# Performance work log

Hardware: AMD Instinct MI355X
Metric: run time of the kernel (lower is better)

The kernel has to match this reference:

```python
import jax
import jax.numpy as jnp
import numpy as np

# Config mirroring GLOBAL_CONFIG['attn'] / kernel config in the source
BM = 64            # query-group (block) size; asserted 64 or 192 in source
TOP_KEYS = 0.1     # fraction of keys kept via top-k on colsum scores
MULTIPLE_OF = 64   # counts_multiple_of: indices_count rounded to this
LW1D = 0.15        # local_1d_window fraction
RAND_INV_PROB = 100

B, H, N, D = 1, 12, 2048, 128


def setup_inputs() -> dict:
    key = jax.random.key(0)
    kq, kk, kv, kc = jax.random.split(key, 4)
    shape = (B, H, N, D)
    q = jax.random.normal(kq, shape, dtype=jnp.float32)
    k = jax.random.normal(kk, shape, dtype=jnp.float32)
    v = jax.random.normal(kv, shape, dtype=jnp.float32)
    out_cache = jax.random.normal(kc, shape, dtype=jnp.float32)
    return {"q": q, "k": k, "v": v, "out_cache": out_cache}


def _static_1d_mask(n: int, bm: int, lw1d: float) -> jnp.ndarray:
    # initialize_1d_static_mask: per query-group local window centered at
    # qg*bm + bm//2, width int(lw1d*n), clipped to [0, n). Shape [qg, n].
    qg = n // bm
    ws = int(lw1d * n)
    centers = jnp.arange(qg) * bm + bm // 2          # [qg]
    j = jnp.arange(n)                                  # [n]
    lo = centers[:, None] - ws // 2
    hi = centers[:, None] + ws // 2
    return (j[None, :] >= lo) & (j[None, :] < hi)


def _scatter_true(mask, idx):
    # mask.scatter_(-1, idx, True) along last axis
    K = idx.shape[-1]
    n = mask.shape[-1]
    flat = mask.reshape(-1, n)
    fidx = idx.reshape(-1, K)
    rows = jnp.arange(flat.shape[0])[:, None]
    flat = flat.at[rows, fidx].set(True)
    return flat.reshape(mask.shape)


def _sparse_diff_attn(q, k, v, out_cache):
    b, h, n, d = q.shape
    qg = n // BM
    scale = 1.0 / jnp.sqrt(jnp.asarray(d, q.dtype))
    # dense scores (dense_colsum_attn computes these on the full step)
    scores = jnp.einsum('bhid,bhjd->bhij', q, k) * scale   # [b,h,n,n]
    probs = jax.nn.softmax(scores, axis=-1)
    # bs: column-sum of attention probabilities per query group  [b,h,qg,n]
    bs = probs.reshape(b, h, qg, BM, n).sum(axis=3)
    # indices_count = multiple_of * round(top_keys * n / multiple_of)
    indices_count = MULTIPLE_OF * int(round(TOP_KEYS * n / MULTIPLE_OF))
    rmask = jax.random.randint(jax.random.key(1), bs.shape, 0, RAND_INV_PROB) == 0
    _, idx = jax.lax.top_k(bs, indices_count)
    mask = _scatter_true(rmask, idx)                       # [b,h,qg,n]
    static = _static_1d_mask(n, BM, LW1D)                  # [qg,n]
    # video_query_groups: groups where static window + topk still sparse
    vqg = (static.sum(axis=-1, keepdims=True) + indices_count) < n  # [qg,1]
    mask = mask & vqg[None, None]
    mask = mask | static[None, None]
    # csp_attn: block-sparse attention; every query i in group i//BM attends
    # only to keys selected in mask[.., i//BM, :]
    full_mask = jnp.repeat(mask, BM, axis=2)               # [b,h,n,n]
    sp_scores = jnp.where(full_mask, scores, -jnp.inf)
    sp_probs = jax.nn.softmax(sp_scores, axis=-1)
    sp_out = jnp.einsum('bhij,bhjd->bhid', sp_probs, v)
    # sparse step: o = o_cache + csp_attn(...)  (sign = +1)
    return out_cache + sp_out


def reference(q, k, v, out_cache):
    return _sparse_diff_attn(q, k, v, out_cache)
```

## Files before the change

### kernel.cpp

```cpp
#include <hip/hip_runtime.h>
#include <math.h>

constexpr int Hh   = 12;
constexpr int Nn   = 2048;
constexpr int Dd   = 128;
constexpr int BMq  = 64;
constexpr int QGg  = 32;
constexpr int KSEL = 192;
constexpr int CK   = 32;
constexpr float SCALE = 0.08838834764831845f;

typedef _Float16 v8h __attribute__((ext_vector_type(8)));
typedef float    v4f __attribute__((ext_vector_type(4)));

__device__ __attribute__((aligned(16))) _Float16 g_qh[(size_t)Hh*Nn*Dd];
__device__ __attribute__((aligned(16))) _Float16 g_ql[(size_t)Hh*Nn*Dd];
__device__ __attribute__((aligned(16))) _Float16 g_kh[(size_t)Hh*Nn*Dd];
__device__ __attribute__((aligned(16))) _Float16 g_kl[(size_t)Hh*Nn*Dd];
__device__ float          g_lp[(size_t)Hh*Nn*16];
__device__ float          g_bs[(size_t)Hh*QGg*Nn];
__device__ unsigned short g_sel[Hh*QGg*Nn];
__device__ int            g_cnt[Hh*QGg];

__device__ __forceinline__ unsigned int rotl32(unsigned int x, int n){
  return (x << n) | (x >> (32 - n));
}

__device__ __forceinline__ unsigned pack2h(_Float16 a, _Float16 b){
  unsigned short ua, ub;
  __builtin_memcpy(&ua, &a, 2);
  __builtin_memcpy(&ub, &b, 2);
  return (unsigned)ua | ((unsigned)ub << 16);
}

__device__ __forceinline__ void tf2x32(unsigned int k0, unsigned int k1,
                                       unsigned int x0, unsigned int x1,
                                       unsigned int &o0, unsigned int &o1){
  const unsigned int ks2 = 0x1BD11BDAu ^ k0 ^ k1;
  x0 += k0; x1 += k1;
  x0 += x1; x1 = rotl32(x1,13); x1 ^= x0;
  x0 += x1; x1 = rotl32(x1,15); x1 ^= x0;
  x0 += x1; x1 = rotl32(x1,26); x1 ^= x0;
  x0 += x1; x1 = rotl32(x1, 6); x1 ^= x0;
  x0 += k1; x1 += ks2 + 1u;
  x0 += x1; x1 = rotl32(x1,17); x1 ^= x0;
  x0 += x1; x1 = rotl32(x1,29); x1 ^= x0;
  x0 += x1; x1 = rotl32(x1,16); x1 ^= x0;
  x0 += x1; x1 = rotl32(x1,24); x1 ^= x0;
  x0 += ks2; x1 += k0 + 2u;
  x0 += x1; x1 = rotl32(x1,13); x1 ^= x0;
  x0 += x1; x1 = rotl32(x1,15); x1 ^= x0;
  x0 += x1; x1 = rotl32(x1,26); x1 ^= x0;
  x0 += x1; x1 = rotl32(x1, 6); x1 ^= x0;
  x0 += k0; x1 += k1 + 3u;
  x0 += x1; x1 = rotl32(x1,17); x1 ^= x0;
  x0 += x1; x1 = rotl32(x1,29); x1 ^= x0;
  x0 += x1; x1 = rotl32(x1,16); x1 ^= x0;
  x0 += x1; x1 = rotl32(x1,24); x1 ^= x0;
  x0 += k1; x1 += ks2 + 4u;
  x0 += x1; x1 = rotl32(x1,13); x1 ^= x0;
  x0 += x1; x1 = rotl32(x1,15); x1 ^= x0;
  x0 += x1; x1 = rotl32(x1,26); x1 ^= x0;
  x0 += x1; x1 = rotl32(x1, 6); x1 ^= x0;
  x0 += ks2; x1 += k0 + 5u;
  o0 = x0; o1 = x1;
}

__device__ __forceinline__ bool jax_rand01(unsigned int idx,
                                           unsigned int k1a, unsigned int k1b,
                                           unsigned int k2a, unsigned int k2b){
  unsigned int h0, h1, l0, l1;
  tf2x32(k1a, k1b, 0u, idx, h0, h1);
  tf2x32(k2a, k2b, 0u, idx, l0, l1);
  unsigned int h = h0 ^ h1;
  unsigned int l = l0 ^ l1;
  unsigned int off = ((h % 100u) * 96u + (l % 100u)) % 100u;
  return off == 0u;
}

__global__ __launch_bounds__(256) void k0_cvt(const float* __restrict__ Q,
                                              const float* __restrict__ K){
  const int bid = blockIdx.x;
  const int t = threadIdx.x;
  const int kc = t >> 6, ln = t & 63;
  const int row = ln & 15;
  const int col = kc*32 + (ln >> 4)*8;
  const size_t src = ((size_t)bid*16 + row)*Dd + col;
  const size_t ob  = (((size_t)bid)*4 + kc)*512 + (size_t)ln*8;

  float4 qa = *(const float4*)(Q + src);
  float4 qb = *(const float4*)(Q + src + 4);
  float qs[8] = {qa.x*SCALE, qa.y*SCALE, qa.z*SCALE, qa.w*SCALE,
                 qb.x*SCALE, qb.y*SCALE, qb.z*SCALE, qb.w*SCALE};
  v8h qh, ql;
  #pragma unroll
  for (int j = 0; j < 8; ++j){
    _Float16 hi = (_Float16)qs[j];
    qh[j] = hi;
    ql[j] = (_Float16)(qs[j] - (float)hi);
  }
  *(v8h*)&g_qh[ob] = qh;
  *(v8h*)&g_ql[ob] = ql;

  float4 ka = *(const float4*)(K + src);
  float4 kb = *(const float4*)(K + src + 4);
  float ks[8] = {ka.x, ka.y, ka.z, ka.w, kb.x, kb.y, kb.z, kb.w};
  v8h kh, kl;
  #pragma unroll
  for (int j = 0; j < 8; ++j){
    _Float16 hi = (_Float16)ks[j];
    kh[j] = hi;
    kl[j] = (_Float16)(ks[j] - (float)hi);
  }
  *(v8h*)&g_kh[ob] = kh;
  *(v8h*)&g_kl[ob] = kl;
}

__global__ __launch_bounds__(256) void k1_rowsum(){
  const int bid0 = blockIdx.x;
  const int w = (bid0 & 7)*384 + (bid0 >> 3);
  const int jb = w & 15, gp = (w >> 4) & 15, h = w >> 8;
  const int t = threadIdx.x;
  const int wv = t >> 6, ln = t & 63;
  const int nidx = ln & 15, quad = ln >> 4;
  const size_t lnoff = (size_t)ln*8;
  const size_t habase = ((size_t)h*128 + gp*8 + wv*2)*4;
  const size_t hbbase = ((size_t)h*128 + jb*8)*4;

  v4f acc[2][8];
  #pragma unroll
  for (int tr = 0; tr < 2; ++tr)
    #pragma unroll
    for (int tc = 0; tc < 8; ++tc)
      acc[tr][tc] = (v4f){0.f, 0.f, 0.f, 0.f};

  for (int kc = 0; kc < 4; ++kc){
    v8h ahi[2], alo[2];
    #pragma unroll
    for (int tr = 0; tr < 2; ++tr){
      const size_t ab = (habase + tr*4 + kc)*512 + lnoff;
      ahi[tr] = *(const v8h*)&g_qh[ab];
      alo[tr] = *(const v8h*)&g_ql[ab];
    }
    v8h bhi[8], blo[8];
    #pragma unroll
    for (int tc = 0; tc < 8; ++tc){
      const size_t bb = (hbbase + tc*4 + kc)*512 + lnoff;
      bhi[tc] = *(const v8h*)&g_kh[bb];
      blo[tc] = *(const v8h*)&g_kl[bb];
    }
    #pragma unroll
    for (int tr = 0; tr < 2; ++tr)
      #pragma unroll
      for (int tc = 0; tc < 8; ++tc){
        acc[tr][tc] = __builtin_amdgcn_mfma_f32_16x16x32_f16(ahi[tr], bhi[tc], acc[tr][tc], 0, 0, 0);
        acc[tr][tc] = __builtin_amdgcn_mfma_f32_16x16x32_f16(ahi[tr], blo[tc], acc[tr][tc], 0, 0, 0);
        acc[tr][tc] = __builtin_amdgcn_mfma_f32_16x16x32_f16(alo[tr], bhi[tc], acc[tr][tc], 0, 0, 0);
      }
  }

  #pragma unroll
  for (int tr = 0; tr < 2; ++tr){
    float rs[4] = {0.f, 0.f, 0.f, 0.f};
    #pragma unroll
    for (int tc = 0; tc < 8; ++tc){
      #pragma unroll
      for (int r = 0; r < 4; ++r){
        rs[r] += __expf(acc[tr][tc][r]);
      }
    }
    #pragma unroll
    for (int r = 0; r < 4; ++r){
      float v = rs[r];
      v += __shfl_xor(v, 1);
      v += __shfl_xor(v, 2);
      v += __shfl_xor(v, 4);
      v += __shfl_xor(v, 8);
      rs[r] = v;
    }
    if (nidx == 0){
      #pragma unroll
      for (int r = 0; r < 4; ++r){
        const int row = (wv*2+tr)*16 + quad*4 + r;
        g_lp[((size_t)h*Nn + gp*128 + row)*16 + jb] = rs[r];
      }
    }
  }
}

__global__ __launch_bounds__(256) void k2r_colsum(){
  const int bid0 = blockIdx.x;
  const int w = (bid0 & 7)*384 + (bid0 >> 3);
  const int jb = w & 15, gp = (w >> 4) & 15, h = w >> 8;
  const int t = threadIdx.x;
  const int wv = t >> 6, ln = t & 63;
  const int nidx = ln & 15, quad = ln >> 4;
  const size_t lnoff = (size_t)ln*8;
  const size_t habase = ((size_t)h*128 + gp*8 + wv*2)*4;
  const size_t hbbase = ((size_t)h*128 + jb*8)*4;

  __shared__ float il_s[128];
  __shared__ float part[4][128];
  if (t < 128){
    const float* lp = &g_lp[((size_t)h*Nn + gp*128 + t)*16];
    float s = 0.f;
    #pragma unroll
    for (int x = 0; x < 16; ++x) s += lp[x];
    il_s[t] = 1.0f / s;
  }
  __syncthreads();

  v4f acc[2][8];
  #pragma unroll
  for (int tr = 0; tr < 2; ++tr)
    #pragma unroll
    for (int tc = 0; tc < 8; ++tc)
      acc[tr][tc] = (v4f){0.f, 0.f, 0.f, 0.f};

  for (int kc = 0; kc < 4; ++kc){
    v8h ahi[2], alo[2];
    #pragma unroll
    for (int tr = 0; tr < 2; ++tr){
      const size_t ab = (habase + tr*4 + kc)*512 + lnoff;
      ahi[tr] = *(const v8h*)&g_qh[ab];
      alo[tr] = *(const v8h*)&g_ql[ab];
    }
    v8h bhi[8], blo[8];
    #pragma unroll
    for (int tc = 0; tc < 8; ++tc){
      const size_t bb = (hbbase + tc*4 + kc)*512 + lnoff;
      bhi[tc] = *(const v8h*)&g_kh[bb];
      blo[tc] = *(const v8h*)&g_kl[bb];
    }
    #pragma unroll
    for (int tr = 0; tr < 2; ++tr)
      #pragma unroll
      for (int tc = 0; tc < 8; ++tc){
        acc[tr][tc] = __builtin_amdgcn_mfma_f32_16x16x32_f16(ahi[tr], bhi[tc], acc[tr][tc], 0, 0, 0);
        acc[tr][tc] = __builtin_amdgcn_mfma_f32_16x16x32_f16(ahi[tr], blo[tc], acc[tr][tc], 0, 0, 0);
        acc[tr][tc] = __builtin_amdgcn_mfma_f32_16x16x32_f16(alo[tr], bhi[tc], acc[tr][tc], 0, 0, 0);
      }
  }

  float csg[8];
  #pragma unroll
  for (int tc = 0; tc < 8; ++tc) csg[tc] = 0.f;
  #pragma unroll
  for (int tr = 0; tr < 2; ++tr){
    #pragma unroll
    for (int tc = 0; tc < 8; ++tc){
      float cs = 0.f;
      #pragma unroll
      for (int r = 0; r < 4; ++r){
        const int row = (wv*2+tr)*16 + quad*4 + r;
        cs += __expf(acc[tr][tc][r]) * il_s[row];
      }
      cs += __shfl_xor(cs, 16);
      cs += __shfl_xor(cs, 32);
      csg[tc] += cs;
    }
  }
  if (ln < 16){
    #pragma unroll
    for (int tc = 0; tc < 8; ++tc) part[wv][tc*16 + nidx] = csg[tc];
  }
  __syncthreads();
  const int col = t & 127, grp = t >> 7;
  g_bs[((size_t)h*QGg + gp*2 + grp)*Nn + jb*128 + col] =
      part[grp*2][col] + part[grp*2 + 1][col];
}

__global__ __launch_bounds__(256) void k2b_mask(){
  const int bid = blockIdx.x, g = bid % QGg, t = threadIdx.x;
  const int wv = t >> 6, lw = t & 63;
  __shared__ int hist[256];
  __shared__ int wsum[4];
  __shared__ int selb_s, selgt_s;
  __shared__ int csel;
  __shared__ int eqn;
  __shared__ int eqpos[Nn];
  const float* src = g_bs + (size_t)bid*Nn;
  float mine[8];
  {
    float4 a = *(const float4*)&src[t*4];
    float4 b = *(const float4*)&src[1024 + t*4];
    mine[0]=a.x; mine[1]=a.y; mine[2]=a.z; mine[3]=a.w;
    mine[4]=b.x; mine[5]=b.y; mine[6]=b.z; mine[7]=b.w;
  }
  if (t == 0){ csel = 0; eqn = 0; }
  unsigned int bu8[8];
  #pragma unroll
  for (int u = 0; u < 8; ++u) bu8[u] = __float_as_uint(mine[u]);

  unsigned int k1a, k1b, k2a, k2b;
  tf2x32(0u, 1u, 0u, 0u, k1a, k1b);
  tf2x32(0u, 1u, 0u, 1u, k2a, k2b);

  unsigned int pref = 0u;
  unsigned int msk  = 0u;
  int rem = KSEL;
  #pragma unroll
  for (int pass = 3; pass >= 0; --pass){
    const int shift = pass*8;
    hist[t] = 0;
    __syncthreads();
    #pragma unroll
    for (int u = 0; u < 8; ++u){
      if ((bu8[u] & msk) == pref)
        atomicAdd(&hist[(bu8[u] >> shift) & 0xFFu], 1);
    }
    __syncthreads();
    const int hcnt = hist[t];
    int s = hcnt;
    #pragma unroll
    for (int d = 1; d < 64; d <<= 1){
      int tmp = __shfl_down(s, d);
      if (lw + d < 64) s += tmp;
    }
    if (lw == 0) wsum[wv] = s;
    __syncthreads();
    int base = 0;
    #pragma unroll
    for (int w2 = 1; w2 < 4; ++w2) if (wv + w2 < 4) base += wsum[wv + w2];
    const int gt_incl = s + base;
    const int gt = gt_incl - hcnt;
    if (gt < rem && gt_incl >= rem){ selb_s = t; selgt_s = gt; }
    __syncthreads();
    pref |= ((unsigned)selb_s) << shift;
    msk  |= 0xFFu << shift;
    rem  -= selgt_s;
  }
  const unsigned int T = pref;
  const int need = rem;

  #pragma unroll
  for (int u = 0; u < 8; ++u){
    int j = (u < 4) ? (t*4 + u) : (1024 + t*4 + u - 4);
    if (bu8[u] == T){
      int s = atomicAdd(&eqn, 1);
      eqpos[s] = j;
    }
  }
  __syncthreads();
  const int en = eqn;

  const int lo = g*BMq + BMq/2 - 153;
  const int hi = g*BMq + BMq/2 + 153;
  const int ssum = ((hi < Nn) ? hi : Nn) - ((lo > 0) ? lo : 0);
  const bool vqg = (ssum + KSEL) < Nn;

  #pragma unroll
  for (int u = 0; u < 8; ++u){
    int j = (u < 4) ? (t*4 + u) : (1024 + t*4 + u - 4);
    unsigned int bu = bu8[u];
    bool topk = bu > T;
    if (!topk && bu == T){
      int tr = 0;
      for (int i = 0; i < en; ++i)
        tr += (eqpos[i] < j) ? 1 : 0;
      topk = (tr < need);
    }
    bool rnd = jax_rand01((unsigned)(bid*Nn + j), k1a, k1b, k2a, k2b);
    bool st  = (j >= lo) && (j < hi);
    bool selb = st || ((rnd || topk) && vqg);
    if (selb){
      int slot = atomicAdd(&csel, 1);
      g_sel[(size_t)bid*Nn + slot] = (unsigned short)j;
    }
  }
  __syncthreads();
  if (t == 0) g_cnt[bid] = csel;
}

__global__ __launch_bounds__(256) void k3_attn(const float* __restrict__ K,
                                               const float* __restrict__ V,
                                               const float* __restrict__ OC,
                                               float* __restrict__ out){
  const int bid0 = blockIdx.x;
  const int w    = (bid0 & 7)*96 + (bid0 >> 3);
  const int half = w & 1;
  const int gg   = w >> 1;
  const int h = gg / QGg, g = gg % QGg;
  const int t = threadIdx.x;
  const int wv = t >> 6, ln = t & 63;
  const int nidx = ln & 15, quad = ln >> 4;
  const int qtile = wv >> 1, kdt = wv & 1;

  __shared__ _Float16 kh_s[CK][136];
  __shared__ _Float16 kl_s[CK][136];
  __shared__ _Float16 vTh[Dd][40];
  __shared__ _Float16 vTl[Dd][40];
  __shared__ _Float16 p_h[32][40];
  __shared__ _Float16 p_l[32][40];
  __shared__ float    l_part[2][32];
  __shared__ float    l_s[32];

  const int c = g_cnt[gg];
  const unsigned short* sel = g_sel + (size_t)gg*Nn;

  const int rb = g*4 + half*2 + qtile;
  v8h aHi[4], aLo[4];
  #pragma unroll
  for (int kc = 0; kc < 4; ++kc){
    const size_t ab = (((size_t)h*128 + rb)*4 + kc)*512 + (size_t)ln*8;
    aHi[kc] = *(const v8h*)&g_qh[ab];
    aLo[kc] = *(const v8h*)&g_ql[ab];
  }

  if (t < 64) l_part[t >> 5][t & 31] = 0.0f;

  float4 kreg[4], vreg[4];
  {
    const int cc0 = (c < CK) ? c : CK;
    #pragma unroll
    for (int it = 0; it < 4; ++it){
      int e = it*256 + t, row = e >> 5, c4 = e & 31;
      int j = (row < cc0) ? (int)sel[row] : 0;
      kreg[it] = ((const float4*)(K + ((size_t)h*Nn + j)*Dd))[c4];
      vreg[it] = ((const float4*)(V + ((size_t)h*Nn + j)*Dd))[c4];
    }
  }

  v4f acc[4];
  #pragma unroll
  for (int dt = 0; dt < 4; ++dt) acc[dt] = (v4f){0.f, 0.f, 0.f, 0.f};

  const int cg = (quad ^ ((nidx >> 2) & 3)) * 8;

  for (int c0 = 0; c0 < c; c0 += CK){
    const int cc = ((c - c0) < CK) ? (c - c0) : CK;
    #pragma unroll
    for (int it = 0; it < 4; ++it){
      int e = it*256 + t, row = e >> 5, c4 = e & 31;
      float4 kv = kreg[it];
      float xs[4] = {kv.x, kv.y, kv.z, kv.w};
      _Float16 hh[4], ll[4];
      #pragma unroll
      for (int m = 0; m < 4; ++m){
        _Float16 hi = (_Float16)xs[m];
        hh[m] = hi;
        ll[m] = (_Float16)(xs[m] - (float)hi);
      }
      *(unsigned*)&kh_s[row][c4*4 + 0] = pack2h(hh[0], hh[1]);
      *(unsigned*)&kh_s[row][c4*4 + 2] = pack2h(hh[2], hh[3]);
      *(unsigned*)&kl_s[row][c4*4 + 0] = pack2h(ll[0], ll[1]);
      *(unsigned*)&kl_s[row][c4*4 + 2] = pack2h(ll[2], ll[3]);
      float4 vv = vreg[it];
      float vs[4] = {vv.x, vv.y, vv.z, vv.w};
      const int swz = row ^ ((c4 & 3) << 3);
      #pragma unroll
      for (int m = 0; m < 4; ++m){
        _Float16 hi = (_Float16)vs[m];
        vTh[c4*4 + m][swz] = hi;
        vTl[c4*4 + m][swz] = (_Float16)(vs[m] - (float)hi);
      }
    }
    __syncthreads();
    {
      const int nc0 = c0 + CK;
      if (nc0 < c){
        const int ncc = ((c - nc0) < CK) ? (c - nc0) : CK;
        #pragma unroll
        for (int it = 0; it < 4; ++it){
          int e = it*256 + t, row = e >> 5, c4 = e & 31;
          int j = (row < ncc) ? (int)sel[nc0 + row] : 0;
          kreg[it] = ((const float4*)(K + ((size_t)h*Nn + j)*Dd))[c4];
          vreg[it] = ((const float4*)(V + ((size_t)h*Nn + j)*Dd))[c4];
        }
      }
    }
    v4f sc = (v4f){0.f, 0.f, 0.f, 0.f};
    #pragma unroll
    for (int kc = 0; kc < 4; ++kc){
      v8h bh = *(const v8h*)&kh_s[kdt*16 + nidx][kc*32 + quad*8];
      v8h bl = *(const v8h*)&kl_s[kdt*16 + nidx][kc*32 + quad*8];
      sc = __builtin_amdgcn_mfma_f32_16x16x32_f16(aHi[kc], bh, sc, 0, 0, 0);
      sc = __builtin_amdgcn_mfma_f32_16x16x32_f16(aHi[kc], bl, sc, 0, 0, 0);
      sc = __builtin_amdgcn_mfma_f32_16x16x32_f16(aLo[kc], bh, sc, 0, 0, 0);
    }
    {
      const int k_loc = kdt*16 + nidx;
      float rs[4];
      #pragma unroll
      for (int r = 0; r < 4; ++r){
        float sv = (k_loc < cc) ? __expf(sc[r]) : 0.f;
        rs[r] = sv;
        _Float16 hi = (_Float16)sv;
        const int row = qtile*16 + quad*4 + r;
        p_h[row][k_loc] = hi;
        p_l[row][k_loc] = (_Float16)(sv - (float)hi);
      }
      #pragma unroll
      for (int r = 0; r < 4; ++r){
        float v = rs[r];
        v += __shfl_xor(v, 1);
        v += __shfl_xor(v, 2);
        v += __shfl_xor(v, 4);
        v += __shfl_xor(v, 8);
        rs[r] = v;
      }
      if (nidx == 0){
        #pragma unroll
        for (int r = 0; r < 4; ++r)
          l_part[kdt][qtile*16 + quad*4 + r] += rs[r];
      }
    }
    __syncthreads();
    {
      v8h ph = *(const v8h*)&p_h[qtile*16 + nidx][quad*8];
      v8h pl = *(const v8h*)&p_l[qtile*16 + nidx][quad*8];
      #pragma unroll
      for (int dt = 0; dt < 4; ++dt){
        const int d = (kdt*4 + dt)*16 + nidx;
        v8h vh = *(const v8h*)&vTh[d][cg];
        v8h vl = *(const v8h*)&vTl[d][cg];
        acc[dt] = __builtin_amdgcn_mfma_f32_16x16x32_f16(ph, vh, acc[dt], 0, 0, 0);
        acc[dt] = __builtin_amdgcn_mfma_f32_16x16x32_f16(ph, vl, acc[dt], 0, 0, 0);
        acc[dt] = __builtin_amdgcn_mfma_f32_16x16x32_f16(pl, vh, acc[dt], 0, 0, 0);
      }
    }
    __syncthreads();
  }

  if (t < 32) l_s[t] = 1.0f / (l_part[0][t] + l_part[1][t]);
  __syncthreads();

  #pragma unroll
  for (int dt = 0; dt < 4; ++dt){
    const int d = (kdt*4 + dt)*16 + nidx;
    #pragma unroll
    for (int r = 0; r < 4; ++r){
      const int row = qtile*16 + quad*4 + r;
      const float il = l_s[row];
      const size_t o = ((size_t)h*Nn + (size_t)g*BMq + half*32 + row)*Dd + d;
      out[o] = acc[dt][r]*il + OC[o];
    }
  }
}

extern "C" void kernel_launch(void* const* d_in, const int* in_sizes, int n_in,
                              void* d_out, int out_size, void* d_ws, size_t ws_size,
                              hipStream_t stream) {
  (void)in_sizes; (void)n_in; (void)out_size; (void)d_ws; (void)ws_size;
  const float* Q  = (const float*)d_in[0];
  const float* K  = (const float*)d_in[1];
  const float* V  = (const float*)d_in[2];
  const float* OC = (const float*)d_in[3];
  float* out = (float*)d_out;
  hipLaunchKernelGGL(k0_cvt,     dim3(Hh*128),   dim3(256), 0, stream, Q, K);
  hipLaunchKernelGGL(k1_rowsum,  dim3(Hh*16*16), dim3(256), 0, stream);
  hipLaunchKernelGGL(k2r_colsum, dim3(Hh*16*16), dim3(256), 0, stream);
  hipLaunchKernelGGL(k2b_mask,   dim3(Hh*QGg),   dim3(256), 0, stream);
  hipLaunchKernelGGL(k3_attn,    dim3(Hh*QGg*2), dim3(256), 0, stream, K, V, OC, out);
}
```

Measured before the change: 270.0 us.

## Stage shared K tiles in LDS with double-buffered register prefetch in QK kernels

In both the rowsum and colsum QK^T kernels, each of the four waves used to load the full K hi/lo fragments from global memory on its own. The block now loads them cooperatively into a double-buffered LDS tile, prefetching the next k-chunk into registers while the current one is computed. This cuts redundant global and L2 traffic by a factor of four and frees registers, at the cost of LDS space and one barrier per chunk. The il_s barrier is folded into the loop barriers, with an extra sync before the colsum epilogue.

```diff
diff --git a/kernel.cpp b/kernel.cpp
--- a/kernel.cpp
+++ b/kernel.cpp
@@ -127,6 +127,19 @@
   const size_t habase = ((size_t)h*128 + gp*8 + wv*2)*4;
   const size_t hbbase = ((size_t)h*128 + jb*8)*4;
 
+  __shared__ v8h Bh[2][8][64], Bl[2][8][64];
+  const int f0 = t*2, f1 = t*2 + 1;
+  const int tc0 = f0 >> 6, bln0 = f0 & 63;
+  const int tc1 = f1 >> 6, bln1 = f1 & 63;
+
+  v8h rbh0, rbh1, rbl0, rbl1;
+  {
+    const size_t a0 = (hbbase + tc0*4 + 0)*512 + (size_t)bln0*8;
+    const size_t a1 = (hbbase + tc1*4 + 0)*512 + (size_t)bln1*8;
+    rbh0 = *(const v8h*)&g_kh[a0]; rbh1 = *(const v8h*)&g_kh[a1];
+    rbl0 = *(const v8h*)&g_kl[a0]; rbl1 = *(const v8h*)&g_kl[a1];
+  }
+
   v4f acc[2][8];
   #pragma unroll
   for (int tr = 0; tr < 2; ++tr)
@@ -135,6 +148,16 @@
       acc[tr][tc] = (v4f){0.f, 0.f, 0.f, 0.f};
 
   for (int kc = 0; kc < 4; ++kc){
+    const int cur = kc & 1;
+    Bh[cur][tc0][bln0] = rbh0; Bh[cur][tc1][bln1] = rbh1;
+    Bl[cur][tc0][bln0] = rbl0; Bl[cur][tc1][bln1] = rbl1;
+    __syncthreads();
+    if (kc < 3){
+      const size_t a0 = (hbbase + tc0*4 + kc+1)*512 + (size_t)bln0*8;
+      const size_t a1 = (hbbase + tc1*4 + kc+1)*512 + (size_t)bln1*8;
+      rbh0 = *(const v8h*)&g_kh[a0]; rbh1 = *(const v8h*)&g_kh[a1];
+      rbl0 = *(const v8h*)&g_kl[a0]; rbl1 = *(const v8h*)&g_kl[a1];
+    }
     v8h ahi[2], alo[2];
     #pragma unroll
     for (int tr = 0; tr < 2; ++tr){
@@ -142,21 +165,17 @@
       ahi[tr] = *(const v8h*)&g_qh[ab];
       alo[tr] = *(const v8h*)&g_ql[ab];
     }
-    v8h bhi[8], blo[8];
     #pragma unroll
     for (int tc = 0; tc < 8; ++tc){
-      const size_t bb = (hbbase + tc*4 + kc)*512 + lnoff;
-      bhi[tc] = *(const v8h*)&g_kh[bb];
-      blo[tc] = *(const v8h*)&g_kl[bb];
-    }
-    #pragma unroll
-    for (int tr = 0; tr < 2; ++tr)
-      #pragma unroll
-      for (int tc = 0; tc < 8; ++tc){
-        acc[tr][tc] = __builtin_amdgcn_mfma_f32_16x16x32_f16(ahi[tr], bhi[tc], acc[tr][tc], 0, 0, 0);
-        acc[tr][tc] = __builtin_amdgcn_mfma_f32_16x16x32_f16(ahi[tr], blo[tc], acc[tr][tc], 0, 0, 0);
-        acc[tr][tc] = __builtin_amdgcn_mfma_f32_16x16x32_f16(alo[tr], bhi[tc], acc[tr][tc], 0, 0, 0);
-      }
+      v8h bh = Bh[cur][tc][ln];
+      v8h bl = Bl[cur][tc][ln];
+      #pragma unroll
+      for (int tr = 0; tr < 2; ++tr){
+        acc[tr][tc] = __builtin_amdgcn_mfma_f32_16x16x32_f16(ahi[tr], bh, acc[tr][tc], 0, 0, 0);
+        acc[tr][tc] = __builtin_amdgcn_mfma_f32_16x16x32_f16(ahi[tr], bl, acc[tr][tc], 0, 0, 0);
+        acc[tr][tc] = __builtin_amdgcn_mfma_f32_16x16x32_f16(alo[tr], bh, acc[tr][tc], 0, 0, 0);
+      }
+    }
   }
 
   #pragma unroll
@@ -199,8 +218,20 @@
   const size_t habase = ((size_t)h*128 + gp*8 + wv*2)*4;
   const size_t hbbase = ((size_t)h*128 + jb*8)*4;
 
+  __shared__ v8h Bh[2][8][64], Bl[2][8][64];
   __shared__ float il_s[128];
   __shared__ float part[4][128];
+  const int f0 = t*2, f1 = t*2 + 1;
+  const int tc0 = f0 >> 6, bln0 = f0 & 63;
+  const int tc1 = f1 >> 6, bln1 = f1 & 63;
+
+  v8h rbh0, rbh1, rbl0, rbl1;
+  {
+    const size_t a0 = (hbbase + tc0*4 + 0)*512 + (size_t)bln0*8;
+    const size_t a1 = (hbbase + tc1*4 + 0)*512 + (size_t)bln1*8;
+    rbh0 = *(const v8h*)&g_kh[a0]; rbh1 = *(const v8h*)&g_kh[a1];
+    rbl0 = *(const v8h*)&g_kl[a0]; rbl1 = *(const v8h*)&g_kl[a1];
+  }
   if (t < 128){
     const float* lp = &g_lp[((size_t)h*Nn + gp*128 + t)*16];
     float s = 0.f;
@@ -208,7 +239,6 @@
     for (int x = 0; x < 16; ++x) s += lp[x];
     il_s[t] = 1.0f / s;
   }
-  __syncthreads();
 
   v4f acc[2][8];
   #pragma unroll
@@ -218,6 +248,16 @@
       acc[tr][tc] = (v4f){0.f, 0.f, 0.f, 0.f};
 
   for (int kc = 0; kc < 4; ++kc){
+    const int cur = kc & 1;
+    Bh[cur][tc0][bln0] = rbh0; Bh[cur][tc1][bln1] = rbh1;
+    Bl[cur][tc0][bln0] = rbl0; Bl[cur][tc1][bln1] = rbl1;
+    __syncthreads();
+    if (kc < 3){
+      const size_t a0 = (hbbase + tc0*4 + kc+1)*512 + (size_t)bln0*8;
+      const size_t a1 = (hbbase + tc1*4 + kc+1)*512 + (size_t)bln1*8;
+      rbh0 = *(const v8h*)&g_kh[a0]; rbh1 = *(const v8h*)&g_kh[a1];
+      rbl0 = *(const v8h*)&g_kl[a0]; rbl1 = *(const v8h*)&g_kl[a1];
+    }
     v8h ahi[2], alo[2];
     #pragma unroll
     for (int tr = 0; tr < 2; ++tr){
@@ -225,23 +265,20 @@
       ahi[tr] = *(const v8h*)&g_qh[ab];
       alo[tr] = *(const v8h*)&g_ql[ab];
     }
-    v8h bhi[8], blo[8];
     #pragma unroll
     for (int tc = 0; tc < 8; ++tc){
-      const size_t bb = (hbbase + tc*4 + kc)*512 + lnoff;
-      bhi[tc] = *(const v8h*)&g_kh[bb];
-      blo[tc] = *(const v8h*)&g_kl[bb];
-    }
-    #pragma unroll
-    for (int tr = 0; tr < 2; ++tr)
-      #pragma unroll
-      for (int tc = 0; tc < 8; ++tc){
-        acc[tr][tc] = __builtin_amdgcn_mfma_f32_16x16x32_f16(ahi[tr], bhi[tc], acc[tr][tc], 0, 0, 0);
-        acc[tr][tc] = __builtin_amdgcn_mfma_f32_16x16x32_f16(ahi[tr], blo[tc], acc[tr][tc], 0, 0, 0);
-        acc[tr][tc] = __builtin_amdgcn_mfma_f32_16x16x32_f16(alo[tr], bhi[tc], acc[tr][tc], 0, 0, 0);
-      }
-  }
-
+      v8h bh = Bh[cur][tc][ln];
+      v8h bl = Bl[cur][tc][ln];
+      #pragma unroll
+      for (int tr = 0; tr < 2; ++tr){
+        acc[tr][tc] = __builtin_amdgcn_mfma_f32_16x16x32_f16(ahi[tr], bh, acc[tr][tc], 0, 0, 0);
+        acc[tr][tc] = __builtin_amdgcn_mfma_f32_16x16x32_f16(ahi[tr], bl, acc[tr][tc], 0, 0, 0);
+        acc[tr][tc] = __builtin_amdgcn_mfma_f32_16x16x32_f16(alo[tr], bh, acc[tr][tc], 0, 0, 0);
+      }
+    }
+  }
+
+  __syncthreads();
   float csg[8];
   #pragma unroll
   for (int tc = 0; tc < 8; ++tc) csg[tc] = 0.f;
```

Result: faster. 262.4 us (-2.8%).
